# Performance work log

Hardware: AMD Instinct MI355X
Metric: run time of the kernel (lower is better)

## Reference

```python
import jax, jax.numpy as jnp
import numpy as np

B, L, V, E = 1024, 2048, 100000, 16
F = 3  # number of interacted features
D = F * E  # 48


def setup_inputs() -> dict:
    key = jax.random.key(0)
    ks = jax.random.split(key, 20)
    inp = {}
    inp['i_goods_id'] = jax.random.randint(ks[0], (B,), 0, V, dtype=jnp.int32)
    inp['i_shop_id'] = jax.random.randint(ks[1], (B,), 0, V, dtype=jnp.int32)
    inp['i_cate_id'] = jax.random.randint(ks[2], (B,), 0, V, dtype=jnp.int32)
    inp['visited_goods_ids'] = jax.random.randint(ks[3], (B, L), 0, V, dtype=jnp.int32)
    inp['visited_shop_ids'] = jax.random.randint(ks[4], (B, L), 0, V, dtype=jnp.int32)
    inp['visited_cate_ids'] = jax.random.randint(ks[5], (B, L), 0, V, dtype=jnp.int32)
    # learned params
    inp['emb_table'] = jax.random.normal(ks[6], (V, E), dtype=jnp.float32) * 0.05
    d_in = 2 * D  # concat(item, pooled) = 96
    inp['W1'] = jax.random.normal(ks[7], (d_in, 200), dtype=jnp.float32) * 0.05
    inp['b1'] = jnp.zeros((200,), jnp.float32)
    inp['g1'] = jnp.ones((200,), jnp.float32)
    inp['beta1'] = jnp.zeros((200,), jnp.float32)
    inp['alpha1'] = jnp.zeros((200,), jnp.float32)
    inp['W2'] = jax.random.normal(ks[8], (200, 80), dtype=jnp.float32) * 0.05
    inp['b2'] = jnp.zeros((80,), jnp.float32)
    inp['g2'] = jnp.ones((80,), jnp.float32)
    inp['beta2'] = jnp.zeros((80,), jnp.float32)
    inp['alpha2'] = jnp.zeros((80,), jnp.float32)
    inp['W3'] = jax.random.normal(ks[9], (80, 2), dtype=jnp.float32) * 0.05
    inp['b3'] = jnp.zeros((2,), jnp.float32)
    return inp


def _layernorm(x, g, b, eps=1e-3):
    m = x.mean(-1, keepdims=True)
    v = x.var(-1, keepdims=True)
    return g * (x - m) * jax.lax.rsqrt(v + eps) + b


def _dice(x, alpha, eps=1e-3):
    # BatchNorm(center=False, scale=False) with batch statistics, then Dice gate
    m = x.mean(0, keepdims=True)
    v = x.var(0, keepdims=True)
    xn = (x - m) * jax.lax.rsqrt(v + eps)
    p = jax.nn.sigmoid(xn)
    return alpha * (1.0 - p) * x + p * x


def reference(emb_table, W1, b1, g1, beta1, alpha1, W2, b2, g2, beta2, alpha2,
              W3, b3, i_goods_id, i_shop_id, i_cate_id,
              visited_goods_ids, visited_shop_ids, visited_cate_ids):
    # item embeddings: [B,3] -> [B,3,E] -> flatten [B, 48]
    item_ids = jnp.stack([i_goods_id, i_shop_id, i_cate_id], axis=1)
    X_item = emb_table[item_ids].reshape(item_ids.shape[0], F * E)
    # series: stack to [B,L,3], embed, reshape to [B,L,48] (same layout as tf.reshape)
    series_ids = jnp.stack([visited_goods_ids, visited_shop_ids, visited_cate_ids], axis=2)
    X_series = emb_table[series_ids].reshape(series_ids.shape[0], series_ids.shape[1], F * E)
    valid_mask = visited_goods_ids != 0
    # inner-product attention pooling
    scores = jnp.einsum('be,ble->bl', X_item, X_series)
    masked_scores = scores * valid_mask.astype(jnp.float32)
    pooled = jnp.einsum('bl,ble->be', masked_scores, X_series)
    X = jnp.concatenate([X_item, pooled], axis=1)  # [B, 96]
    h = _dice(_layernorm(X @ W1 + b1, g1, beta1), alpha1)
    h = _dice(_layernorm(h @ W2 + b2, g2, beta2), alpha2)
    output = jax.nn.softmax(h @ W3 + b3, axis=-1)
    return output, X_series, valid_mask
```

## Files before the change

kernel.cpp:

```cpp
#include <hip/hip_runtime.h>
#include <math.h>
#include <stddef.h>

#define BB 1024
#define LL 2048
#define EE 16
#define DD 48
#define N1 200
#define N2 80
#define NSPLIT 8
#define PPB (LL / NSPLIT)
#define POS_PER_IT 64
#define ITERS (PPB / POS_PER_IT)

__global__ __launch_bounds__(256, 6) void pool_kernel(
    const int* __restrict__ ig, const int* __restrict__ ish, const int* __restrict__ ic,
    const int* __restrict__ vg, const int* __restrict__ vs, const int* __restrict__ vc,
    const float* __restrict__ emb,
    float* __restrict__ Xs,
    float* __restrict__ Msk,
    float* __restrict__ X,
    float* __restrict__ P)
{
    const int b   = blockIdx.x;
    const int s   = blockIdx.y;
    const int tid = threadIdx.x;
    const int q   = tid & 3;
    const int pl  = tid >> 2;

    __shared__ float item[DD];
    if (tid < DD) {
        int f = tid >> 4, e = tid & 15;
        int id = (f == 0) ? ig[b] : (f == 1) ? ish[b] : ic[b];
        float v = emb[(size_t)id * EE + e];
        item[tid] = v;
        if (s == 0) X[(size_t)b * 96 + tid] = v;
    }
    __syncthreads();

    float4 it4[3];
#pragma unroll
    for (int f = 0; f < 3; ++f) it4[f] = ((const float4*)item)[f * 4 + q];

    const float4* __restrict__ emb4 = (const float4*)emb;
    const int base = s * PPB;
    const int* vgb = vg + (size_t)b * LL + base;
    const int* vsb = vs + (size_t)b * LL + base;
    const int* vcb = vc + (size_t)b * LL + base;
    float4* __restrict__ Xs4 = (float4*)(Xs + (size_t)b * LL * DD) + (size_t)base * 12;
    float* mb = Msk + (size_t)b * LL + base;

    int pg[ITERS], ps[ITERS], pc[ITERS];
#pragma unroll
    for (int it = 0; it < ITERS; ++it) {
        const int l = it * POS_PER_IT + pl;
        pg[it] = vgb[l]; ps[it] = vsb[l]; pc[it] = vcb[l];
    }

    float pooled[12];
#pragma unroll
    for (int j = 0; j < 12; ++j) pooled[j] = 0.f;

#pragma unroll
    for (int it = 0; it < ITERS; ++it) {
        const int l = it * POS_PER_IT + pl;
        float4 v0 = emb4[(size_t)pg[it] * 4 + q];
        float4 v1 = emb4[(size_t)ps[it] * 4 + q];
        float4 v2 = emb4[(size_t)pc[it] * 4 + q];

        float sc = v0.x * it4[0].x + v0.y * it4[0].y + v0.z * it4[0].z + v0.w * it4[0].w
                 + v1.x * it4[1].x + v1.y * it4[1].y + v1.z * it4[1].z + v1.w * it4[1].w
                 + v2.x * it4[2].x + v2.y * it4[2].y + v2.z * it4[2].z + v2.w * it4[2].w;
        sc += __shfl_xor(sc, 1);
        sc += __shfl_xor(sc, 2);

        const float valid = (pg[it] != 0) ? 1.f : 0.f;
        if (q == 0) mb[l] = valid;
        const float sm = sc * valid;

        const size_t o = (size_t)l * 12 + q;
        Xs4[o]     = v0;
        Xs4[o + 4] = v1;
        Xs4[o + 8] = v2;

        pooled[0] += sm * v0.x; pooled[1]  += sm * v0.y; pooled[2]  += sm * v0.z; pooled[3]  += sm * v0.w;
        pooled[4] += sm * v1.x; pooled[5]  += sm * v1.y; pooled[6]  += sm * v1.z; pooled[7]  += sm * v1.w;
        pooled[8] += sm * v2.x; pooled[9]  += sm * v2.y; pooled[10] += sm * v2.z; pooled[11] += sm * v2.w;
    }

#pragma unroll
    for (int j = 0; j < 12; ++j) {
        float v = pooled[j];
        v += __shfl_xor(v, 4);
        v += __shfl_xor(v, 8);
        v += __shfl_xor(v, 16);
        v += __shfl_xor(v, 32);
        pooled[j] = v;
    }

    __shared__ float wsum[4][DD];
    const int wave = tid >> 6;
    if (pl == 0 || (tid & 63) < 4) {  }
    if ((tid & 63) < 4) {
#pragma unroll
        for (int f = 0; f < 3; ++f)
#pragma unroll
            for (int e = 0; e < 4; ++e)
                wsum[wave][f * 16 + q * 4 + e] = pooled[f * 4 + e];
    }
    __syncthreads();
    if (tid < DD) {
        float sv = wsum[0][tid] + wsum[1][tid] + wsum[2][tid] + wsum[3][tid];
        P[((size_t)b * NSPLIT + s) * DD + tid] = sv;
    }
}

__global__ __launch_bounds__(256) void mlp1_kernel(
    const float* __restrict__ X, const float* __restrict__ P,
    const float* __restrict__ W1,
    const float* __restrict__ b1, const float* __restrict__ g1, const float* __restrict__ be1,
    float* __restrict__ H1)
{
    const int b = blockIdx.x, tid = threadIdx.x;
    __shared__ float xr[96];
    if (tid < DD) {
        xr[tid] = X[(size_t)b * 96 + tid];
    } else if (tid < 96) {
        const int j = tid - DD;
        const float* pp = P + (size_t)b * NSPLIT * DD + j;
        float sv = 0.f;
#pragma unroll
        for (int s = 0; s < NSPLIT; ++s) sv += pp[s * DD];
        xr[tid] = sv;
    }
    __syncthreads();

    float y = 0.f;
    if (tid < N1) {
        y = b1[tid];
        for (int k = 0; k < 96; ++k) y += xr[k] * W1[k * N1 + tid];
    }

    __shared__ float red[256], red2[256];
    float yy = (tid < N1) ? y : 0.f;
    red[tid] = yy; red2[tid] = yy * yy;
    __syncthreads();
    for (int s = 128; s; s >>= 1) {
        if (tid < s) { red[tid] += red[tid + s]; red2[tid] += red2[tid + s]; }
        __syncthreads();
    }
    __shared__ float msh, ish;
    if (tid == 0) {
        float m = red[0] / (float)N1;
        float v = red2[0] / (float)N1 - m * m;
        msh = m; ish = rsqrtf(v + 1e-3f);
    }
    __syncthreads();
    if (tid < N1) H1[(size_t)b * N1 + tid] = g1[tid] * (y - msh) * ish + be1[tid];
}

__global__ __launch_bounds__(256) void colstats_kernel(
    const float* __restrict__ H, int n, int rows,
    float* __restrict__ mout, float* __restrict__ isout)
{
    const int f = blockIdx.x, tid = threadIdx.x;
    float s = 0.f, s2 = 0.f;
    for (int r = tid; r < rows; r += 256) {
        float v = H[(size_t)r * n + f];
        s += v; s2 += v * v;
    }
    __shared__ float red[256], red2[256];
    red[tid] = s; red2[tid] = s2;
    __syncthreads();
    for (int st = 128; st; st >>= 1) {
        if (tid < st) { red[tid] += red[tid + st]; red2[tid] += red2[tid + st]; }
        __syncthreads();
    }
    if (tid == 0) {
        float m = red[0] / (float)rows;
        float v = red2[0] / (float)rows - m * m;
        mout[f] = m;
        isout[f] = rsqrtf(v + 1e-3f);
    }
}

__global__ __launch_bounds__(256) void mlp2_kernel(
    const float* __restrict__ H1, const float* __restrict__ m1, const float* __restrict__ is1,
    const float* __restrict__ a1,
    const float* __restrict__ W2, const float* __restrict__ b2, const float* __restrict__ g2,
    const float* __restrict__ be2,
    float* __restrict__ H2)
{
    const int b = blockIdx.x, tid = threadIdx.x;
    __shared__ float d1[N1];
    if (tid < N1) {
        float h  = H1[(size_t)b * N1 + tid];
        float xn = (h - m1[tid]) * is1[tid];
        float p  = 1.f / (1.f + expf(-xn));
        d1[tid]  = h * (p + a1[tid] * (1.f - p));
    }
    __syncthreads();

    float y = 0.f;
    if (tid < N2) {
        y = b2[tid];
        for (int k = 0; k < N1; ++k) y += d1[k] * W2[k * N2 + tid];
    }

    __shared__ float red[256], red2[256];
    float yy = (tid < N2) ? y : 0.f;
    red[tid] = yy; red2[tid] = yy * yy;
    __syncthreads();
    for (int s = 128; s; s >>= 1) {
        if (tid < s) { red[tid] += red[tid + s]; red2[tid] += red2[tid + s]; }
        __syncthreads();
    }
    __shared__ float msh, ish;
    if (tid == 0) {
        float m = red[0] / (float)N2;
        float v = red2[0] / (float)N2 - m * m;
        msh = m; ish = rsqrtf(v + 1e-3f);
    }
    __syncthreads();
    if (tid < N2) H2[(size_t)b * N2 + tid] = g2[tid] * (y - msh) * ish + be2[tid];
}

__global__ __launch_bounds__(256) void head_kernel(
    const float* __restrict__ H2, const float* __restrict__ m2, const float* __restrict__ is2,
    const float* __restrict__ a2,
    const float* __restrict__ W3, const float* __restrict__ b3,
    float* __restrict__ out)
{
    const int b = blockIdx.x * 256 + threadIdx.x;
    if (b >= BB) return;
    float z0 = b3[0], z1 = b3[1];
    for (int k = 0; k < N2; ++k) {
        float h  = H2[(size_t)b * N2 + k];
        float xn = (h - m2[k]) * is2[k];
        float p  = 1.f / (1.f + expf(-xn));
        float d  = h * (p + a2[k] * (1.f - p));
        z0 += d * W3[k * 2 + 0];
        z1 += d * W3[k * 2 + 1];
    }
    float mx = fmaxf(z0, z1);
    float e0 = expf(z0 - mx), e1 = expf(z1 - mx);
    float inv = 1.f / (e0 + e1);
    out[(size_t)b * 2 + 0] = e0 * inv;
    out[(size_t)b * 2 + 1] = e1 * inv;
}

extern "C" void kernel_launch(void* const* d_in, const int* in_sizes, int n_in,
                              void* d_out, int out_size, void* d_ws, size_t ws_size,
                              hipStream_t stream) {
    const int*   ig  = (const int*)  d_in[0];
    const int*   ish = (const int*)  d_in[1];
    const int*   ic  = (const int*)  d_in[2];
    const int*   vg  = (const int*)  d_in[3];
    const int*   vs  = (const int*)  d_in[4];
    const int*   vc  = (const int*)  d_in[5];
    const float* emb = (const float*)d_in[6];
    const float* W1  = (const float*)d_in[7];
    const float* b1  = (const float*)d_in[8];
    const float* g1  = (const float*)d_in[9];
    const float* be1 = (const float*)d_in[10];
    const float* a1  = (const float*)d_in[11];
    const float* W2  = (const float*)d_in[12];
    const float* b2  = (const float*)d_in[13];
    const float* g2  = (const float*)d_in[14];
    const float* be2 = (const float*)d_in[15];
    const float* a2  = (const float*)d_in[16];
    const float* W3  = (const float*)d_in[17];
    const float* b3  = (const float*)d_in[18];

    float* out  = (float*)d_out;
    float* Xs   = out + (size_t)BB * 2;
    float* Msk  = Xs + (size_t)BB * LL * DD;

    float* X    = (float*)d_ws;
    float* P    = X + (size_t)BB * 96;
    float* H1   = P + (size_t)BB * NSPLIT * DD;
    float* H2v  = H1 + (size_t)BB * N1;
    float* m1   = H2v + (size_t)BB * N2;
    float* is1  = m1 + N1;
    float* m2   = is1 + N1;
    float* is2  = m2 + N2;

    pool_kernel<<<dim3(BB, NSPLIT), 256, 0, stream>>>(ig, ish, ic, vg, vs, vc, emb,
                                                      Xs, Msk, X, P);
    mlp1_kernel<<<BB, 256, 0, stream>>>(X, P, W1, b1, g1, be1, H1);
    colstats_kernel<<<N1, 256, 0, stream>>>(H1, N1, BB, m1, is1);
    mlp2_kernel<<<BB, 256, 0, stream>>>(H1, m1, is1, a1, W2, b2, g2, be2, H2v);
    colstats_kernel<<<N2, 256, 0, stream>>>(H2v, N2, BB, m2, is2);
    head_kernel<<<(BB + 255) / 256, 256, 0, stream>>>(H2v, m2, is2, a2, W3, b3, out);
}
```

Before: 210.3 us.

## Fuse column statistics into MLP kernels via fixed-point 64-bit atomics

Removes the two separate column-statistics kernels by having each row kernel atomically accumulate fixed-point sums and sums of squares into 64-bit integer accumulators. The accumulators are zeroed at the start of the pooling kernel, and the next layer's kernel converts them to mean and inverse std. Fixed-point integer atomics keep the result deterministic but add many global atomics on a small set of addresses, and they carry a precision and overflow risk from the chosen scales.

```diff
diff --git a/kernel.cpp b/kernel.cpp
--- a/kernel.cpp
+++ b/kernel.cpp
@@ -13,6 +13,9 @@
 #define POS_PER_IT 64
 #define ITERS (PPB / POS_PER_IT)
 
+#define S_SUM 4294967296.0
+#define S_SQ  268435456.0
+
 __global__ __launch_bounds__(256, 6) void pool_kernel(
     const int* __restrict__ ig, const int* __restrict__ ish, const int* __restrict__ ic,
     const int* __restrict__ vg, const int* __restrict__ vs, const int* __restrict__ vc,
@@ -20,13 +23,18 @@
     float* __restrict__ Xs,
     float* __restrict__ Msk,
     float* __restrict__ X,
-    float* __restrict__ P)
+    float* __restrict__ P,
+    unsigned long long* __restrict__ acc)
 {
     const int b   = blockIdx.x;
     const int s   = blockIdx.y;
     const int tid = threadIdx.x;
     const int q   = tid & 3;
     const int pl  = tid >> 2;
+
+    if (b == 0 && s == 0) {
+        for (int i = tid; i < 2 * (N1 + N2); i += 256) acc[i] = 0ull;
+    }
 
     __shared__ float item[DD];
     if (tid < DD) {
@@ -100,7 +108,6 @@
 
     __shared__ float wsum[4][DD];
     const int wave = tid >> 6;
-    if (pl == 0 || (tid & 63) < 4) {  }
     if ((tid & 63) < 4) {
 #pragma unroll
         for (int f = 0; f < 3; ++f)
@@ -115,11 +122,11 @@
     }
 }
 
-__global__ __launch_bounds__(256) void mlp1_kernel(
+__global__ __launch_bounds__(256) void t1_kernel(
     const float* __restrict__ X, const float* __restrict__ P,
-    const float* __restrict__ W1,
-    const float* __restrict__ b1, const float* __restrict__ g1, const float* __restrict__ be1,
-    float* __restrict__ H1)
+    const float* __restrict__ W1, const float* __restrict__ b1,
+    const float* __restrict__ g1, const float* __restrict__ be1,
+    float* __restrict__ H1, unsigned long long* __restrict__ acc1)
 {
     const int b = blockIdx.x, tid = threadIdx.x;
     __shared__ float xr[96];
@@ -156,46 +163,34 @@
         msh = m; ish = rsqrtf(v + 1e-3f);
     }
     __syncthreads();
-    if (tid < N1) H1[(size_t)b * N1 + tid] = g1[tid] * (y - msh) * ish + be1[tid];
-}
-
-__global__ __launch_bounds__(256) void colstats_kernel(
-    const float* __restrict__ H, int n, int rows,
-    float* __restrict__ mout, float* __restrict__ isout)
-{
-    const int f = blockIdx.x, tid = threadIdx.x;
-    float s = 0.f, s2 = 0.f;
-    for (int r = tid; r < rows; r += 256) {
-        float v = H[(size_t)r * n + f];
-        s += v; s2 += v * v;
-    }
-    __shared__ float red[256], red2[256];
-    red[tid] = s; red2[tid] = s2;
-    __syncthreads();
-    for (int st = 128; st; st >>= 1) {
-        if (tid < st) { red[tid] += red[tid + st]; red2[tid] += red2[tid + st]; }
-        __syncthreads();
-    }
-    if (tid == 0) {
-        float m = red[0] / (float)rows;
-        float v = red2[0] / (float)rows - m * m;
-        mout[f] = m;
-        isout[f] = rsqrtf(v + 1e-3f);
-    }
-}
-
-__global__ __launch_bounds__(256) void mlp2_kernel(
-    const float* __restrict__ H1, const float* __restrict__ m1, const float* __restrict__ is1,
+    if (tid < N1) {
+        float h = g1[tid] * (y - msh) * ish + be1[tid];
+        H1[(size_t)b * N1 + tid] = h;
+        long long si  = llrint((double)h * S_SUM);
+        long long sqi = llrint((double)(h * h) * S_SQ);
+        atomicAdd(&acc1[tid],      (unsigned long long)si);
+        atomicAdd(&acc1[N1 + tid], (unsigned long long)sqi);
+    }
+}
+
+__global__ __launch_bounds__(256) void t2_kernel(
+    const float* __restrict__ H1, const unsigned long long* __restrict__ acc1,
     const float* __restrict__ a1,
-    const float* __restrict__ W2, const float* __restrict__ b2, const float* __restrict__ g2,
-    const float* __restrict__ be2,
-    float* __restrict__ H2)
+    const float* __restrict__ W2, const float* __restrict__ b2,
+    const float* __restrict__ g2, const float* __restrict__ be2,
+    float* __restrict__ H2, unsigned long long* __restrict__ acc2)
 {
     const int b = blockIdx.x, tid = threadIdx.x;
     __shared__ float d1[N1];
     if (tid < N1) {
+        double s  = (double)(long long)acc1[tid]      * (1.0 / S_SUM);
+        double s2 = (double)(long long)acc1[N1 + tid] * (1.0 / S_SQ);
+        double m  = s / (double)BB;
+        float  vv = (float)(s2 / (double)BB - m * m);
+        float  is = rsqrtf(vv + 1e-3f);
+        float  mf = (float)m;
         float h  = H1[(size_t)b * N1 + tid];
-        float xn = (h - m1[tid]) * is1[tid];
+        float xn = (h - mf) * is;
         float p  = 1.f / (1.f + expf(-xn));
         d1[tid]  = h * (p + a1[tid] * (1.f - p));
     }
@@ -222,21 +217,40 @@
         msh = m; ish = rsqrtf(v + 1e-3f);
     }
     __syncthreads();
-    if (tid < N2) H2[(size_t)b * N2 + tid] = g2[tid] * (y - msh) * ish + be2[tid];
-}
-
-__global__ __launch_bounds__(256) void head_kernel(
-    const float* __restrict__ H2, const float* __restrict__ m2, const float* __restrict__ is2,
+    if (tid < N2) {
+        float h = g2[tid] * (y - msh) * ish + be2[tid];
+        H2[(size_t)b * N2 + tid] = h;
+        long long si  = llrint((double)h * S_SUM);
+        long long sqi = llrint((double)(h * h) * S_SQ);
+        atomicAdd(&acc2[tid],      (unsigned long long)si);
+        atomicAdd(&acc2[N2 + tid], (unsigned long long)sqi);
+    }
+}
+
+__global__ __launch_bounds__(256) void t3_kernel(
+    const float* __restrict__ H2, const unsigned long long* __restrict__ acc2,
     const float* __restrict__ a2,
     const float* __restrict__ W3, const float* __restrict__ b3,
     float* __restrict__ out)
 {
-    const int b = blockIdx.x * 256 + threadIdx.x;
+    const int tid = threadIdx.x;
+    __shared__ float m2s[N2], is2s[N2];
+    if (tid < N2) {
+        double s  = (double)(long long)acc2[tid]      * (1.0 / S_SUM);
+        double s2 = (double)(long long)acc2[N2 + tid] * (1.0 / S_SQ);
+        double m  = s / (double)BB;
+        float  vv = (float)(s2 / (double)BB - m * m);
+        m2s[tid]  = (float)m;
+        is2s[tid] = rsqrtf(vv + 1e-3f);
+    }
+    __syncthreads();
+
+    const int b = blockIdx.x * 256 + tid;
     if (b >= BB) return;
     float z0 = b3[0], z1 = b3[1];
     for (int k = 0; k < N2; ++k) {
         float h  = H2[(size_t)b * N2 + k];
-        float xn = (h - m2[k]) * is2[k];
+        float xn = (h - m2s[k]) * is2s[k];
         float p  = 1.f / (1.f + expf(-xn));
         float d  = h * (p + a2[k] * (1.f - p));
         z0 += d * W3[k * 2 + 0];
@@ -280,16 +294,12 @@
     float* P    = X + (size_t)BB * 96;
     float* H1   = P + (size_t)BB * NSPLIT * DD;
     float* H2v  = H1 + (size_t)BB * N1;
-    float* m1   = H2v + (size_t)BB * N2;
-    float* is1  = m1 + N1;
-    float* m2   = is1 + N1;
-    float* is2  = m2 + N2;
+    unsigned long long* acc1 = (unsigned long long*)(H2v + (size_t)BB * N2);
+    unsigned long long* acc2 = acc1 + 2 * N1;
 
     pool_kernel<<<dim3(BB, NSPLIT), 256, 0, stream>>>(ig, ish, ic, vg, vs, vc, emb,
-                                                      Xs, Msk, X, P);
-    mlp1_kernel<<<BB, 256, 0, stream>>>(X, P, W1, b1, g1, be1, H1);
-    colstats_kernel<<<N1, 256, 0, stream>>>(H1, N1, BB, m1, is1);
-    mlp2_kernel<<<BB, 256, 0, stream>>>(H1, m1, is1, a1, W2, b2, g2, be2, H2v);
-    colstats_kernel<<<N2, 256, 0, stream>>>(H2v, N2, BB, m2, is2);
-    head_kernel<<<(BB + 255) / 256, 256, 0, stream>>>(H2v, m2, is2, a2, W3, b3, out);
-}
+                                                      Xs, Msk, X, P, acc1);
+    t1_kernel<<<BB, 256, 0, stream>>>(X, P, W1, b1, g1, be1, H1, acc1);
+    t2_kernel<<<BB, 256, 0, stream>>>(H1, acc1, a1, W2, b2, g2, be2, H2v, acc2);
+    t3_kernel<<<(BB + 255) / 256, 256, 0, stream>>>(H2v, acc2, a2, W3, b3, out);
+}
```

New measurement: 243.8 us. +15.9%, slower.
